# Kernel optimization log

Hardware: AMD Instinct MI355X
Metric: run time of the kernel (lower is better)

Reference implementation:

```python
import jax, jax.numpy as jnp
import numpy as np

B, L, DIM, S, K = 2, 2048, 1024, 16, 3
INNER = DIM  # expand = 1 (module only runs with expand=1, see notes)


def setup_inputs() -> dict:
    key = jax.random.key(0)
    ks = jax.random.split(key, 10)
    f = lambda k, shape, s=0.02: jax.random.normal(k, shape, jnp.float32) * s
    return {
        "x": jax.random.normal(ks[0], (B, L, DIM), jnp.float32),
        "gamma": jnp.ones((DIM,), jnp.float32),
        "beta": jnp.zeros((DIM,), jnp.float32),
        "W_in": f(ks[1], (2 * INNER, DIM)),
        "conv_w": f(ks[2], (INNER, 1, K), 0.2),   # depthwise conv, OIL layout
        "W_x": f(ks[3], (2 * S, INNER)),
        "W_dt": f(ks[4], (INNER, DIM)),
        "b_dt": f(ks[5], (INNER,), 0.1),
        "A_log": jax.random.normal(ks[6], (INNER, S), jnp.float32),
        "D_param": jnp.ones((INNER,), jnp.float32),
        "W_out": f(ks[7], (DIM, INNER)),
    }


def reference(x, gamma, beta, W_in, conv_w, W_x, W_dt, b_dt, A_log, D_param, W_out):
    residual = x
    # LayerNorm
    mu = jnp.mean(x, axis=-1, keepdims=True)
    var = jnp.var(x, axis=-1, keepdims=True)
    h = (x - mu) / jnp.sqrt(var + 1e-5) * gamma + beta
    # in_proj + chunk
    xz = jnp.einsum('bld,ed->ble', h, W_in)
    inner = W_in.shape[0] // 2
    xx, z = xz[..., :inner], xz[..., inner:]
    # depthwise conv1d, padding (K-1)//2, no bias
    k = conv_w.shape[-1]
    pad = (k - 1) // 2
    xc = jax.lax.conv_general_dilated(
        xx.transpose(0, 2, 1), conv_w, window_strides=(1,),
        padding=[(pad, pad)], dimension_numbers=('NCL', 'OIL', 'NCL'),
        feature_group_count=inner).transpose(0, 2, 1)
    xc = jax.nn.silu(xc)
    # projections for dt, B, C
    dt = jnp.einsum('bld,ed->ble', xc, W_dt) + b_dt
    BC = jnp.einsum('bld,ed->ble', xc, W_x)
    s = A_log.shape[-1]
    Bm, Cm = BC[..., :s], BC[..., s:]
    # selective scan
    A = -jnp.exp(A_log)                               # (d, s)
    dt = jax.nn.softplus(dt)                          # (b, l, d)
    dA = jnp.exp(jnp.einsum('bld,ds->blds', dt, A))   # (b, l, d, s)
    dB = jnp.einsum('bld,bls->blds', dt, Bm)          # (b, l, d, s)

    def step(state, inputs):
        dA_t, dB_t, C_t = inputs                      # (b,d,s), (b,d,s), (b,s)
        state = state * dA_t + dB_t
        y_t = jnp.einsum('bds,bs->bd', state, C_t)
        return state, y_t

    init = jnp.zeros((x.shape[0], inner, s), xc.dtype)
    _, ys = jax.lax.scan(
        step, init,
        (dA.transpose(1, 0, 2, 3), dB.transpose(1, 0, 2, 3), Cm.transpose(1, 0, 2)))
    y = ys.transpose(1, 0, 2)                         # (b, l, d)
    # skip, gate, out projection, residual
    y = y + D_param * xc
    y = y * jax.nn.silu(z)
    out = jnp.einsum('bld,ed->ble', y, W_out)
    return out + residual
```

## Files before the change

kernel.cpp:

```cpp
#include <hip/hip_runtime.h>
#include <math.h>

#define BB 2
#define LL 2048
#define DIMV 1024
#define SSV 16
#define INNERV 1024
#define E2V 2048
#define MMV (BB*LL)
#define NCHUNK 64
#define CLEN 32

typedef __attribute__((ext_vector_type(8))) short short8;
typedef __attribute__((ext_vector_type(4))) float f32x4;

static __device__ __forceinline__ float4 ld4(const float* p){
  return *reinterpret_cast<const float4*>(p);
}
static __device__ __forceinline__ ushort f2bf(float x){
  unsigned u = __float_as_uint(x);
  unsigned r = (u + 0x7fffu + ((u >> 16) & 1u)) >> 16;
  return (ushort)r;
}
static __device__ __forceinline__ float bf2f(ushort h){
  return __uint_as_float(((unsigned)h) << 16);
}
static __device__ __forceinline__ void gld16(const void* g, void* l){
  __builtin_amdgcn_global_load_lds(
      (const __attribute__((address_space(1))) void*)g,
      (__attribute__((address_space(3))) void*)l, 16, 0, 0);
}

__global__ __launch_bounds__(256) void ln_init(
        const float* __restrict__ x, const float* __restrict__ gamma,
        const float* __restrict__ beta, ushort* __restrict__ hh,
        const float* __restrict__ W_in, const float* __restrict__ W_dt,
        const float* __restrict__ W_out, const float* __restrict__ wx,
        ushort* __restrict__ Wih, ushort* __restrict__ Wch,
        ushort* __restrict__ Woh){
  __shared__ float red[8];
  if (blockIdx.x < 4224){
    int idx = blockIdx.x*256 + threadIdx.x;
    if (idx < 1032*1024){
      const float* src; ushort* dst; int i;
      if (idx < 512*1024){ src = W_in;  dst = Wih; i = idx; }
      else if (idx < 768*1024){ src = W_dt;  dst = Wch; i = idx - 512*1024; }
      else if (idx < 1024*1024){ src = W_out; dst = Woh; i = idx - 768*1024; }
      else { src = wx; dst = Wch + (size_t)1024*1024; i = idx - 1024*1024; }
      float4 v = ld4(src + (size_t)i*4);
      ushort4 H;
      H.x=f2bf(v.x); H.y=f2bf(v.y); H.z=f2bf(v.z); H.w=f2bf(v.w);
      *reinterpret_cast<ushort4*>(dst + (size_t)i*4) = H;
    } else {
      int i = idx - 1032*1024;
      *reinterpret_cast<ushort4*>(Wch + (size_t)1056*1024 + (size_t)i*4) =
          make_ushort4(0,0,0,0);
    }
    return;
  }
  int row = blockIdx.x - 4224;
  int tid = threadIdx.x;
  const float* xr = x + (size_t)row*DIMV;
  float4 v = ld4(xr + tid*4);
  float s  = v.x+v.y+v.z+v.w;
  float s2 = v.x*v.x+v.y*v.y+v.z*v.z+v.w*v.w;
  for (int o=32;o;o>>=1){ s += __shfl_down(s,o); s2 += __shfl_down(s2,o); }
  int wid = tid>>6, lane = tid&63;
  if (lane==0){ red[wid]=s; red[4+wid]=s2; }
  __syncthreads();
  s  = red[0]+red[1]+red[2]+red[3];
  s2 = red[4]+red[5]+red[6]+red[7];
  float mu  = s*(1.f/DIMV);
  float var = s2*(1.f/DIMV) - mu*mu;
  float rstd = rsqrtf(var + 1e-5f);
  float4 g = ld4(gamma + tid*4), be = ld4(beta + tid*4);
  ushort4 H;
  H.x = f2bf((v.x-mu)*rstd*g.x + be.x);
  H.y = f2bf((v.y-mu)*rstd*g.y + be.y);
  H.z = f2bf((v.z-mu)*rstd*g.z + be.z);
  H.w = f2bf((v.w-mu)*rstd*g.w + be.w);
  *reinterpret_cast<ushort4*>(hh + (size_t)row*DIMV + tid*4) = H;
}

#define GBK 64
#define NKT 16

template<int EPI>
static __device__ __forceinline__ void gemm_body(ushort* lds,
    const ushort* __restrict__ A, const ushort* __restrict__ Bw,
    void* __restrict__ Co_, int N, const float* __restrict__ aux,
    float* __restrict__ aux2, int bm, int bn){
  const int t  = threadIdx.x;
  const int rr  = t >> 3;
  const int k16 = (t & 7) ^ (rr & 7);
  const ushort* gA = A  + (size_t)(bm + rr)*1024 + k16*8;
  const ushort* gB = Bw + (size_t)(bn + rr)*1024 + k16*8;
  const int wofs = (t >> 6) * 1024;

  const int l  = t & 63, wv = t >> 6;
  const int wm = wv & 1, wn = wv >> 1;
  const int fr = l & 15, kb = l >> 4;

  f32x4 acc[2][2];
  #pragma unroll
  for (int m=0;m<2;m++){
    #pragma unroll
    for (int n=0;n<2;n++) acc[m][n] = (f32x4){0.f,0.f,0.f,0.f};
  }

  char* Lb = (char*)lds;
  for (int kt = 0; kt < NKT; ++kt){
    const int ko = kt*GBK;
    gld16(gA + ko,           Lb +     0 + wofs);
    gld16(gA + ko + 32*1024, Lb +  4096 + wofs);
    gld16(gB + ko,           Lb +  8192 + wofs);
    gld16(gB + ko + 32*1024, Lb + 12288 + wofs);
    __syncthreads();
    short8 a[2][2], b[2][2];
    #pragma unroll
    for (int m=0;m<2;m++){
      int row = wm*32 + m*16 + fr;
      #pragma unroll
      for (int ks=0;ks<2;ks++)
        a[m][ks] = *(const short8*)(Lb + row*128 + (((ks*4+kb)^(fr&7))*16));
    }
    #pragma unroll
    for (int n=0;n<2;n++){
      int row = wn*32 + n*16 + fr;
      #pragma unroll
      for (int ks=0;ks<2;ks++)
        b[n][ks] = *(const short8*)(Lb + 8192 + row*128 + (((ks*4+kb)^(fr&7))*16));
    }
    #pragma unroll
    for (int ks=0;ks<2;ks++){
      #pragma unroll
      for (int m=0;m<2;m++){
        #pragma unroll
        for (int n=0;n<2;n++)
          acc[m][n] = __builtin_amdgcn_mfma_f32_16x16x32_bf16(a[m][ks], b[n][ks], acc[m][n], 0,0,0);
      }
    }
    __syncthreads();
  }

  #pragma unroll
  for (int m=0;m<2;m++){
    int row0 = bm + wm*32 + m*16 + kb*4;
    #pragma unroll
    for (int n=0;n<2;n++){
      int col = bn + wn*32 + n*16 + fr;
      #pragma unroll
      for (int j=0;j<4;j++){
        int r = row0 + j;
        float v = acc[m][n][j];
        if (EPI==0){
          ((ushort*)Co_)[(size_t)r*N + col] = f2bf(v);
        } else if (EPI==2){
          v += aux[(size_t)r*N + col];
          ((float*)Co_)[(size_t)r*N + col] = v;
        } else {
          if (col < 1024){
            v += aux[col];
            v = (v > 20.f) ? v : log1pf(__expf(v));
            ((ushort*)Co_)[(size_t)r*1024 + col] = f2bf(v);
          } else if (col < 1056){
            aux2[(size_t)r*32 + (col - 1024)] = v;
          }
        }
      }
    }
  }
}

template<int EPI>
__global__ __launch_bounds__(256, 6) void gemm_bf16(
    const ushort* __restrict__ A, const ushort* __restrict__ Bw,
    void* __restrict__ Co_, int N, const float* __restrict__ aux){
  __shared__ __align__(16) ushort lds[8192];
  gemm_body<EPI>(lds, A, Bw, Co_, N, aux, nullptr, blockIdx.y*64, blockIdx.x*64);
}

__global__ __launch_bounds__(256, 6) void gemm_dtbc(
    const ushort* __restrict__ xch, const ushort* __restrict__ Wch,
    ushort* __restrict__ dtb, const float* __restrict__ b_dt,
    float* __restrict__ bcb){
  __shared__ __align__(16) ushort lds[8192];
  gemm_body<3>(lds, xch, Wch, dtb, 1024, b_dt, bcb, blockIdx.y*64, blockIdx.x*64);
}

__global__ __launch_bounds__(256) void conv_silu_kernel(const ushort* __restrict__ xz,
        const float* __restrict__ cw, ushort* __restrict__ xch){
  int idx = blockIdx.x*256 + threadIdx.x;
  int d4  = idx & 255;
  int row = idx >> 8;
  int t = row & (LL-1);
  const ushort* p = xz + (size_t)row*E2V + d4*4;
  ushort4 u1 = *reinterpret_cast<const ushort4*>(p);
  ushort4 u0 = (t>0)    ? *reinterpret_cast<const ushort4*>(p - E2V) : make_ushort4(0,0,0,0);
  ushort4 u2 = (t<LL-1) ? *reinterpret_cast<const ushort4*>(p + E2V) : make_ushort4(0,0,0,0);
  int d = d4*4;
  float w[12];
  #pragma unroll
  for (int i=0;i<12;i++) w[i] = cw[d*3 + i];
  float4 o;
  o.x = bf2f(u0.x)*w[0] + bf2f(u1.x)*w[1]  + bf2f(u2.x)*w[2];
  o.y = bf2f(u0.y)*w[3] + bf2f(u1.y)*w[4]  + bf2f(u2.y)*w[5];
  o.z = bf2f(u0.z)*w[6] + bf2f(u1.z)*w[7]  + bf2f(u2.z)*w[8];
  o.w = bf2f(u0.w)*w[9] + bf2f(u1.w)*w[10] + bf2f(u2.w)*w[11];
  o.x = o.x / (1.f + __expf(-o.x));
  o.y = o.y / (1.f + __expf(-o.y));
  o.z = o.z / (1.f + __expf(-o.z));
  o.w = o.w / (1.f + __expf(-o.w));
  ushort4 H;
  H.x=f2bf(o.x); H.y=f2bf(o.y); H.z=f2bf(o.z); H.w=f2bf(o.w);
  *reinterpret_cast<ushort4*>(xch + (size_t)row*DIMV + d4*4) = H;
}

__global__ __launch_bounds__(256) void scan_p1(const ushort* __restrict__ dt,
        const float* __restrict__ bc, const float* __restrict__ A_log,
        ushort* __restrict__ F, ushort* __restrict__ P){
  __shared__ float sB[CLEN*32];
  int bid = blockIdx.x;
  int dblk = bid & 3;
  int c  = (bid >> 2) & (NCHUNK-1);
  int b  = bid >> 8;
  int tid = threadIdx.x;
  int d = dblk*256 + tid;
  int row0 = b*LL + c*CLEN;
  ((float4*)sB)[tid] = *((const float4*)(bc + (size_t)row0*32) + tid);
  float a[16];
  {
    const float4* ap = (const float4*)(A_log + d*16);
    #pragma unroll
    for (int q=0;q<4;q++){
      float4 v = ap[q];
      a[q*4+0]=-__expf(v.x); a[q*4+1]=-__expf(v.y);
      a[q*4+2]=-__expf(v.z); a[q*4+3]=-__expf(v.w);
    }
  }
  __syncthreads();
  float st[16];
  #pragma unroll
  for (int s=0;s<16;s++) st[s]=0.f;
  float sdt = 0.f;
  const ushort* dtp = dt + (size_t)row0*DIMV + d;
  for (int t=0;t<CLEN;t++){
    float dtv = bf2f(dtp[(size_t)t*DIMV]);
    sdt += dtv;
    float4 B0 = *(const float4*)&sB[t*32+0];
    float4 B1 = *(const float4*)&sB[t*32+4];
    float4 B2 = *(const float4*)&sB[t*32+8];
    float4 B3 = *(const float4*)&sB[t*32+12];
    float Bv[16] = {B0.x,B0.y,B0.z,B0.w,B1.x,B1.y,B1.z,B1.w,
                    B2.x,B2.y,B2.z,B2.w,B3.x,B3.y,B3.z,B3.w};
    #pragma unroll
    for (int s=0;s<16;s++){
      float dA = __expf(dtv*a[s]);
      st[s] = fmaf(st[s], dA, dtv*Bv[s]);
    }
  }
  size_t o = ((size_t)((b*NCHUNK + c)*DIMV + d))*16;
  #pragma unroll
  for (int q=0;q<4;q++){
    ushort4 fv, pv;
    fv.x=f2bf(st[q*4]);   fv.y=f2bf(st[q*4+1]);
    fv.z=f2bf(st[q*4+2]); fv.w=f2bf(st[q*4+3]);
    pv.x=f2bf(__expf(sdt*a[q*4]));   pv.y=f2bf(__expf(sdt*a[q*4+1]));
    pv.z=f2bf(__expf(sdt*a[q*4+2])); pv.w=f2bf(__expf(sdt*a[q*4+3]));
    *(ushort4*)(F + o + q*4) = fv;
    *(ushort4*)(P + o + q*4) = pv;
  }
}

__global__ __launch_bounds__(256) void scan_p2(const ushort* __restrict__ F,
        const ushort* __restrict__ P, ushort* __restrict__ E){
  int idx = blockIdx.x*256 + threadIdx.x;
  int b  = idx >> 14;
  int ds = idx & 16383;
  float e = 0.f;
  for (int c=0;c<NCHUNK;c++){
    size_t o = ((size_t)(b*NCHUNK + c) << 14) + ds;
    E[o] = f2bf(e);
    e = fmaf(bf2f(P[o]), e, bf2f(F[o]));
  }
}

__global__ __launch_bounds__(256) void scan_p3(const ushort* __restrict__ dt,
        const float* __restrict__ bc, const float* __restrict__ A_log,
        const ushort* __restrict__ E, const ushort* __restrict__ xch,
        const ushort* __restrict__ xz, const float* __restrict__ Dp,
        ushort* __restrict__ yh){
  __shared__ float sBC[CLEN*32];
  int bid = blockIdx.x;
  int dblk = bid & 3;
  int c  = (bid >> 2) & (NCHUNK-1);
  int b  = bid >> 8;
  int tid = threadIdx.x;
  int d = dblk*256 + tid;
  int row0 = b*LL + c*CLEN;
  ((float4*)sBC)[tid] = *((const float4*)(bc + (size_t)row0*32) + tid);
  float a[16];
  {
    const float4* ap = (const float4*)(A_log + d*16);
    #pragma unroll
    for (int q=0;q<4;q++){
      float4 v = ap[q];
      a[q*4+0]=-__expf(v.x); a[q*4+1]=-__expf(v.y);
      a[q*4+2]=-__expf(v.z); a[q*4+3]=-__expf(v.w);
    }
  }
  float st[16];
  {
    size_t o = ((size_t)((b*NCHUNK + c)*DIMV + d))*16;
    #pragma unroll
    for (int q=0;q<4;q++){
      ushort4 v = *(const ushort4*)(E + o + q*4);
      st[q*4]=bf2f(v.x); st[q*4+1]=bf2f(v.y); st[q*4+2]=bf2f(v.z); st[q*4+3]=bf2f(v.w);
    }
  }
  float Dv = Dp[d];
  __syncthreads();
  const ushort* dtp = dt + (size_t)row0*DIMV + d;
  for (int t=0;t<CLEN;t++){
    float dtv = bf2f(dtp[(size_t)t*DIMV]);
    float4 B0 = *(const float4*)&sBC[t*32+0];
    float4 B1 = *(const float4*)&sBC[t*32+4];
    float4 B2 = *(const float4*)&sBC[t*32+8];
    float4 B3 = *(const float4*)&sBC[t*32+12];
    float4 C0 = *(const float4*)&sBC[t*32+16];
    float4 C1 = *(const float4*)&sBC[t*32+20];
    float4 C2 = *(const float4*)&sBC[t*32+24];
    float4 C3 = *(const float4*)&sBC[t*32+28];
    float Bv[16] = {B0.x,B0.y,B0.z,B0.w,B1.x,B1.y,B1.z,B1.w,
                    B2.x,B2.y,B2.z,B2.w,B3.x,B3.y,B3.z,B3.w};
    float Cv[16] = {C0.x,C0.y,C0.z,C0.w,C1.x,C1.y,C1.z,C1.w,
                    C2.x,C2.y,C2.z,C2.w,C3.x,C3.y,C3.z,C3.w};
    float y = 0.f;
    #pragma unroll
    for (int s=0;s<16;s++){
      float dA = __expf(dtv*a[s]);
      st[s] = fmaf(st[s], dA, dtv*Bv[s]);
      y = fmaf(st[s], Cv[s], y);
    }
    int row = row0 + t;
    size_t ofs = (size_t)row*DIMV + d;
    float xcv = bf2f(xch[ofs]);
    float zv  = bf2f(xz[(size_t)row*E2V + INNERV + d]);
    float sz  = zv / (1.f + __expf(-zv));
    yh[ofs] = f2bf((y + Dv*xcv)*sz);
  }
}

extern "C" void kernel_launch(void* const* d_in, const int* in_sizes, int n_in,
                              void* d_out, int out_size, void* d_ws, size_t ws_size,
                              hipStream_t stream){
  const float* x     = (const float*)d_in[0];
  const float* gamma = (const float*)d_in[1];
  const float* beta  = (const float*)d_in[2];
  const float* W_in  = (const float*)d_in[3];
  const float* cw    = (const float*)d_in[4];
  const float* W_x   = (const float*)d_in[5];
  const float* W_dt  = (const float*)d_in[6];
  const float* b_dt  = (const float*)d_in[7];
  const float* A_log = (const float*)d_in[8];
  const float* Dp    = (const float*)d_in[9];
  const float* W_out = (const float*)d_in[10];
  float* out = (float*)d_out;
  float* ws  = (float*)d_ws;
  const size_t MB = (size_t)1 << 20;
  ushort* xzh = (ushort*)ws;
  ushort* hh  = (ushort*)(ws + 4*MB);
  ushort* yh  = (ushort*)(ws + 4*MB);
  ushort* xch = (ushort*)(ws + 6*MB);
  ushort* dtb = (ushort*)(ws + 8*MB);
  ushort* F   = (ushort*)(ws + 10*MB);
  ushort* P   = (ushort*)(ws + 11*MB);
  ushort* E   = (ushort*)(ws + 12*MB);
  ushort* Wih = (ushort*)(ws + 13*MB);
  ushort* Wch = (ushort*)(ws + 14*MB);
  ushort* Woh = (ushort*)(ws + 14*MB + 640*1024);
  float*  bcb = ws + 15*MB + 256*1024;

  ln_init<<<4224 + MMV, 256, 0, stream>>>(x, gamma, beta, hh,
                                          W_in, W_dt, W_out, W_x,
                                          Wih, Wch, Woh);
  gemm_bf16<0><<<dim3(E2V/64, MMV/64), 256, 0, stream>>>(hh, Wih, xzh, E2V, nullptr);
  conv_silu_kernel<<<(MMV*(DIMV/4))/256, 256, 0, stream>>>(xzh, cw, xch);
  gemm_dtbc<<<dim3(18, MMV/64), 256, 0, stream>>>(xch, Wch, dtb, b_dt, bcb);
  scan_p1<<<BB*NCHUNK*(DIMV/256), 256, 0, stream>>>(dtb, bcb, A_log, F, P);
  scan_p2<<<(BB*DIMV*SSV)/256, 256, 0, stream>>>(F, P, E);
  scan_p3<<<BB*NCHUNK*(DIMV/256), 256, 0, stream>>>(dtb, bcb, A_log, E, xch, xzh, Dp, yh);
  gemm_bf16<2><<<dim3(DIMV/64, MMV/64), 256, 0, stream>>>(yh, Woh, out, DIMV, x);
}
```

Baseline: 152.6 us.

## Double-buffer LDS tiles in bf16 GEMM to overlap loads with MFMA

Result: slower. 156.6 us (+2.6%).

```diff
diff --git a/kernel.cpp b/kernel.cpp
--- a/kernel.cpp
+++ b/kernel.cpp
@@ -108,40 +108,57 @@
     for (int n=0;n<2;n++) acc[m][n] = (f32x4){0.f,0.f,0.f,0.f};
   }
 
-  char* Lb = (char*)lds;
-  for (int kt = 0; kt < NKT; ++kt){
-    const int ko = kt*GBK;
-    gld16(gA + ko,           Lb +     0 + wofs);
-    gld16(gA + ko + 32*1024, Lb +  4096 + wofs);
-    gld16(gB + ko,           Lb +  8192 + wofs);
-    gld16(gB + ko + 32*1024, Lb + 12288 + wofs);
+  char* Lb0 = (char*)lds;
+  char* Lb1 = (char*)lds + 16384;
+
+  #define STAGE_T(base, kt_) { \
+    const int ko = (kt_)*GBK; \
+    gld16(gA + ko,           (base) +     0 + wofs); \
+    gld16(gA + ko + 32*1024, (base) +  4096 + wofs); \
+    gld16(gB + ko,           (base) +  8192 + wofs); \
+    gld16(gB + ko + 32*1024, (base) + 12288 + wofs); }
+
+  #define COMPUTE_T(base) { \
+    short8 a[2][2], b[2][2]; \
+    _Pragma("unroll") \
+    for (int m=0;m<2;m++){ \
+      int row = wm*32 + m*16 + fr; \
+      _Pragma("unroll") \
+      for (int ks=0;ks<2;ks++) \
+        a[m][ks] = *(const short8*)((base) + row*128 + (((ks*4+kb)^(fr&7))*16)); \
+    } \
+    _Pragma("unroll") \
+    for (int n=0;n<2;n++){ \
+      int row = wn*32 + n*16 + fr; \
+      _Pragma("unroll") \
+      for (int ks=0;ks<2;ks++) \
+        b[n][ks] = *(const short8*)((base) + 8192 + row*128 + (((ks*4+kb)^(fr&7))*16)); \
+    } \
+    _Pragma("unroll") \
+    for (int ks=0;ks<2;ks++){ \
+      _Pragma("unroll") \
+      for (int m=0;m<2;m++){ \
+        _Pragma("unroll") \
+        for (int n=0;n<2;n++) \
+          acc[m][n] = __builtin_amdgcn_mfma_f32_16x16x32_bf16(a[m][ks], b[n][ks], acc[m][n], 0,0,0); \
+      } \
+    } }
+
+  STAGE_T(Lb0, 0);
+  __syncthreads();
+  #pragma unroll 1
+  for (int kt = 0; kt < NKT; kt += 2){
+    if (kt+1 < NKT) STAGE_T(Lb1, kt+1);
+    COMPUTE_T(Lb0);
     __syncthreads();
-    short8 a[2][2], b[2][2];
-    #pragma unroll
-    for (int m=0;m<2;m++){
-      int row = wm*32 + m*16 + fr;
-      #pragma unroll
-      for (int ks=0;ks<2;ks++)
-        a[m][ks] = *(const short8*)(Lb + row*128 + (((ks*4+kb)^(fr&7))*16));
-    }
-    #pragma unroll
-    for (int n=0;n<2;n++){
-      int row = wn*32 + n*16 + fr;
-      #pragma unroll
-      for (int ks=0;ks<2;ks++)
-        b[n][ks] = *(const short8*)(Lb + 8192 + row*128 + (((ks*4+kb)^(fr&7))*16));
-    }
-    #pragma unroll
-    for (int ks=0;ks<2;ks++){
-      #pragma unroll
-      for (int m=0;m<2;m++){
-        #pragma unroll
-        for (int n=0;n<2;n++)
-          acc[m][n] = __builtin_amdgcn_mfma_f32_16x16x32_bf16(a[m][ks], b[n][ks], acc[m][n], 0,0,0);
-      }
-    }
-    __syncthreads();
-  }
+    if (kt+1 < NKT){
+      if (kt+2 < NKT) STAGE_T(Lb0, kt+2);
+      COMPUTE_T(Lb1);
+      __syncthreads();
+    }
+  }
+  #undef STAGE_T
+  #undef COMPUTE_T
 
   #pragma unroll
   for (int m=0;m<2;m++){
@@ -173,18 +190,18 @@
 }
 
 template<int EPI>
-__global__ __launch_bounds__(256, 6) void gemm_bf16(
+__global__ __launch_bounds__(256, 4) void gemm_bf16(
     const ushort* __restrict__ A, const ushort* __restrict__ Bw,
     void* __restrict__ Co_, int N, const float* __restrict__ aux){
-  __shared__ __align__(16) ushort lds[8192];
+  __shared__ __align__(16) ushort lds[16384];
   gemm_body<EPI>(lds, A, Bw, Co_, N, aux, nullptr, blockIdx.y*64, blockIdx.x*64);
 }
 
-__global__ __launch_bounds__(256, 6) void gemm_dtbc(
+__global__ __launch_bounds__(256, 4) void gemm_dtbc(
     const ushort* __restrict__ xch, const ushort* __restrict__ Wch,
     ushort* __restrict__ dtb, const float* __restrict__ b_dt,
     float* __restrict__ bcb){
-  __shared__ __align__(16) ushort lds[8192];
+  __shared__ __align__(16) ushort lds[16384];
   gemm_body<3>(lds, xch, Wch, dtb, 1024, b_dt, bcb, blockIdx.y*64, blockIdx.x*64);
 }
 
```

## Replace 64x64 four-wave GEMM tiles with 32x32 single-wave tiles and XCD swizzle

Applied to the files above, without the earlier changes.

Measured after the change: 201.9 us. +32.3%, slower.

```diff
diff --git a/kernel.cpp b/kernel.cpp
--- a/kernel.cpp
+++ b/kernel.cpp
@@ -29,6 +29,14 @@
   __builtin_amdgcn_global_load_lds(
       (const __attribute__((address_space(1))) void*)g,
       (__attribute__((address_space(3))) void*)l, 16, 0, 0);
+}
+
+static __device__ __forceinline__ int xcd_swz(){
+  int bid = blockIdx.x;
+  int nwg = gridDim.x;
+  int q = nwg >> 3, r = nwg & 7;
+  int xcd = bid & 7, idx = bid >> 3;
+  return (xcd < r ? xcd*(q+1) : r*(q+1) + (xcd - r)*q) + idx;
 }
 
 __global__ __launch_bounds__(256) void ln_init(
@@ -82,24 +90,24 @@
   *reinterpret_cast<ushort4*>(hh + (size_t)row*DIMV + tid*4) = H;
 }
 
-#define GBK 64
-#define NKT 16
+#define NKT32 32
 
 template<int EPI>
-static __device__ __forceinline__ void gemm_body(ushort* lds,
+__global__ __launch_bounds__(64, 8) void gemm_w(
     const ushort* __restrict__ A, const ushort* __restrict__ Bw,
     void* __restrict__ Co_, int N, const float* __restrict__ aux,
-    float* __restrict__ aux2, int bm, int bn){
-  const int t  = threadIdx.x;
-  const int rr  = t >> 3;
-  const int k16 = (t & 7) ^ (rr & 7);
-  const ushort* gA = A  + (size_t)(bm + rr)*1024 + k16*8;
-  const ushort* gB = Bw + (size_t)(bn + rr)*1024 + k16*8;
-  const int wofs = (t >> 6) * 1024;
-
-  const int l  = t & 63, wv = t >> 6;
-  const int wm = wv & 1, wn = wv >> 1;
-  const int fr = l & 15, kb = l >> 4;
+    float* __restrict__ aux2, int ncol){
+  __shared__ __align__(16) ushort lds[2048];
+  int wg = xcd_swz();
+  int bm = (wg / ncol)*32, bn = (wg % ncol)*32;
+
+  const int t = threadIdx.x;
+  const int rowc = t >> 2;
+  const int lu = (t & 3) ^ (rowc & 3);
+  const ushort* gA = A  + (size_t)(bm + rowc)*1024 + lu*8;
+  const ushort* gB = Bw + (size_t)(bn + rowc)*1024 + lu*8;
+  const int fr = t & 15, kb = t >> 4;
+  const int sw = ((kb ^ (fr & 3)) * 16);
 
   f32x4 acc[2][2];
   #pragma unroll
@@ -109,46 +117,35 @@
   }
 
   char* Lb = (char*)lds;
-  for (int kt = 0; kt < NKT; ++kt){
-    const int ko = kt*GBK;
-    gld16(gA + ko,           Lb +     0 + wofs);
-    gld16(gA + ko + 32*1024, Lb +  4096 + wofs);
-    gld16(gB + ko,           Lb +  8192 + wofs);
-    gld16(gB + ko + 32*1024, Lb + 12288 + wofs);
+  for (int kt = 0; kt < NKT32; ++kt){
+    const int ko = kt*32;
+    gld16(gA + ko,            Lb +    0);
+    gld16(gA + ko + 16*1024,  Lb + 1024);
+    gld16(gB + ko,            Lb + 2048);
+    gld16(gB + ko + 16*1024,  Lb + 3072);
     __syncthreads();
-    short8 a[2][2], b[2][2];
+    short8 a[2], b[2];
+    #pragma unroll
+    for (int m=0;m<2;m++)
+      a[m] = *(const short8*)(Lb + (m*16 + fr)*64 + sw);
+    #pragma unroll
+    for (int n=0;n<2;n++)
+      b[n] = *(const short8*)(Lb + 2048 + (n*16 + fr)*64 + sw);
     #pragma unroll
     for (int m=0;m<2;m++){
-      int row = wm*32 + m*16 + fr;
       #pragma unroll
-      for (int ks=0;ks<2;ks++)
-        a[m][ks] = *(const short8*)(Lb + row*128 + (((ks*4+kb)^(fr&7))*16));
-    }
+      for (int n=0;n<2;n++)
+        acc[m][n] = __builtin_amdgcn_mfma_f32_16x16x32_bf16(a[m], b[n], acc[m][n], 0,0,0);
+    }
+    __syncthreads();
+  }
+
+  #pragma unroll
+  for (int m=0;m<2;m++){
+    int row0 = bm + m*16 + kb*4;
     #pragma unroll
     for (int n=0;n<2;n++){
-      int row = wn*32 + n*16 + fr;
-      #pragma unroll
-      for (int ks=0;ks<2;ks++)
-        b[n][ks] = *(const short8*)(Lb + 8192 + row*128 + (((ks*4+kb)^(fr&7))*16));
-    }
-    #pragma unroll
-    for (int ks=0;ks<2;ks++){
-      #pragma unroll
-      for (int m=0;m<2;m++){
-        #pragma unroll
-        for (int n=0;n<2;n++)
-          acc[m][n] = __builtin_amdgcn_mfma_f32_16x16x32_bf16(a[m][ks], b[n][ks], acc[m][n], 0,0,0);
-      }
-    }
-    __syncthreads();
-  }
-
-  #pragma unroll
-  for (int m=0;m<2;m++){
-    int row0 = bm + wm*32 + m*16 + kb*4;
-    #pragma unroll
-    for (int n=0;n<2;n++){
-      int col = bn + wn*32 + n*16 + fr;
+      int col = bn + n*16 + fr;
       #pragma unroll
       for (int j=0;j<4;j++){
         int r = row0 + j;
@@ -170,22 +167,6 @@
       }
     }
   }
-}
-
-template<int EPI>
-__global__ __launch_bounds__(256, 6) void gemm_bf16(
-    const ushort* __restrict__ A, const ushort* __restrict__ Bw,
-    void* __restrict__ Co_, int N, const float* __restrict__ aux){
-  __shared__ __align__(16) ushort lds[8192];
-  gemm_body<EPI>(lds, A, Bw, Co_, N, aux, nullptr, blockIdx.y*64, blockIdx.x*64);
-}
-
-__global__ __launch_bounds__(256, 6) void gemm_dtbc(
-    const ushort* __restrict__ xch, const ushort* __restrict__ Wch,
-    ushort* __restrict__ dtb, const float* __restrict__ b_dt,
-    float* __restrict__ bcb){
-  __shared__ __align__(16) ushort lds[8192];
-  gemm_body<3>(lds, xch, Wch, dtb, 1024, b_dt, bcb, blockIdx.y*64, blockIdx.x*64);
 }
 
 __global__ __launch_bounds__(256) void conv_silu_kernel(const ushort* __restrict__ xz,
@@ -384,11 +365,11 @@
   ln_init<<<4224 + MMV, 256, 0, stream>>>(x, gamma, beta, hh,
                                           W_in, W_dt, W_out, W_x,
                                           Wih, Wch, Woh);
-  gemm_bf16<0><<<dim3(E2V/64, MMV/64), 256, 0, stream>>>(hh, Wih, xzh, E2V, nullptr);
+  gemm_w<0><<<8192, 64, 0, stream>>>(hh, Wih, xzh, E2V, nullptr, nullptr, 64);
   conv_silu_kernel<<<(MMV*(DIMV/4))/256, 256, 0, stream>>>(xzh, cw, xch);
-  gemm_dtbc<<<dim3(18, MMV/64), 256, 0, stream>>>(xch, Wch, dtb, b_dt, bcb);
+  gemm_w<3><<<4224, 64, 0, stream>>>(xch, Wch, dtb, 1024, b_dt, bcb, 33);
   scan_p1<<<BB*NCHUNK*(DIMV/256), 256, 0, stream>>>(dtb, bcb, A_log, F, P);
   scan_p2<<<(BB*DIMV*SSV)/256, 256, 0, stream>>>(F, P, E);
   scan_p3<<<BB*NCHUNK*(DIMV/256), 256, 0, stream>>>(dtb, bcb, A_log, E, xch, xzh, Dp, yh);
-  gemm_bf16<2><<<dim3(DIMV/64, MMV/64), 256, 0, stream>>>(yh, Woh, out, DIMV, x);
-}
+  gemm_w<2><<<4096, 64, 0, stream>>>(yh, Woh, out, DIMV, x, nullptr, 32);
+}
```
